# Optimization experiments

Measured on AMD Instinct MI355X. Metric: run time of the kernel, lower is better.

Reference implementation:

```python
import jax, jax.numpy as jnp
import numpy as np

HEADS = 8
DIM_HEAD = 64
SCALE = DIM_HEAD ** -0.5


def setup_inputs() -> dict:
    key = jax.random.key(0)
    ks = jax.random.split(key, 6)
    B, T, C, H, W = 16, 64, 512, 64, 64
    inner = HEADS * DIM_HEAD  # 512
    return {
        "vision_feature": jax.random.normal(ks[0], (B, C, H, W), jnp.float32),
        "language_feature": jax.random.normal(ks[1], (B, T, C), jnp.float32),
        "mask": jnp.ones((B, T), jnp.int32),  # unused by the module's forward
        "Wq": jax.random.normal(ks[2], (inner, C), jnp.float32) * (C ** -0.5),
        "Wk": jax.random.normal(ks[3], (inner, C), jnp.float32) * (C ** -0.5),
        "Wv": jax.random.normal(ks[4], (inner, C), jnp.float32) * (C ** -0.5),
        "Wo": jax.random.normal(ks[5], (C, inner), jnp.float32) * (inner ** -0.5),
    }


def reference(vision_feature, language_feature, mask, Wq, Wk, Wv, Wo):
    B, T, C = language_feature.shape
    _, _, H, W = vision_feature.shape
    S = H * W
    # 1x1 conv projections == matmuls over the channel dim
    q = jnp.einsum('btc,ic->bti', language_feature, Wq)           # (B, T, inner)
    vis = vision_feature.reshape(B, C, S)                          # (B, C, S)
    k = jnp.einsum('ic,bcs->bis', Wk, vis)                         # (B, inner, S)
    v = jnp.einsum('ic,bcs->bis', Wv, vis)                         # (B, inner, S)
    # split heads: channel index = n*dim_head + d  (n outermost)
    q = q.reshape(B, T, HEADS, DIM_HEAD).transpose(2, 0, 1, 3)     # (h, B, T, d)
    k = k.reshape(B, HEADS, DIM_HEAD, S).transpose(1, 0, 2, 3)     # (h, B, d, S)
    v = v.reshape(B, HEADS, DIM_HEAD, S).transpose(1, 0, 3, 2)     # (h, B, S, d)
    att = jax.nn.softmax(jnp.einsum('hbtd,hbds->hbts', q, k) * SCALE, axis=-1)
    out = jnp.einsum('hbts,hbsd->hbtd', att, v)                    # (h, B, T, d)
    # merge heads back: b (n c) tokens -> equivalently (B, T, h*d)
    out = out.transpose(1, 2, 0, 3).reshape(B, T, HEADS * DIM_HEAD)
    out = jnp.einsum('bti,oi->bto', out, Wo)                       # (B, T, C)
    return out
```

## Files before the change

### kernel.cpp

```cpp
#include <hip/hip_runtime.h>
#include <stdint.h>

typedef __attribute__((ext_vector_type(8))) short short8;
typedef __attribute__((ext_vector_type(4))) short short4v;
typedef __attribute__((ext_vector_type(4))) float float4v;
typedef __attribute__((ext_vector_type(8))) __bf16 bf16x8;

#define NCH 4

__device__ __forceinline__ float4v mfma16x16x32(short8 a, short8 b, float4v c) {
  return __builtin_amdgcn_mfma_f32_16x16x32_bf16(
      __builtin_bit_cast(bf16x8, a), __builtin_bit_cast(bf16x8, b), c, 0, 0, 0);
}

__device__ __forceinline__ short f2bf(float f) {
  uint32_t u = __builtin_bit_cast(uint32_t, f);
  u += 0x7fffu + ((u >> 16) & 1u);
  return (short)(u >> 16);
}

__device__ __forceinline__ float bf2f(short s) {
  return __builtin_bit_cast(float, ((uint32_t)(uint16_t)s) << 16);
}

__device__ __forceinline__ void load_lds16(const short* g, short* l) {
  __builtin_amdgcn_global_load_lds(
      (const __attribute__((address_space(1))) void*)g,
      (__attribute__((address_space(3))) void*)l, 16, 0, 0);
}

__global__ __launch_bounds__(256) void convert5(
    const float* __restrict__ sl, short* __restrict__ dl,
    const float* __restrict__ s1, short* __restrict__ d1,
    const float* __restrict__ s2, short* __restrict__ d2,
    const float* __restrict__ s3, short* __restrict__ d3,
    const float* __restrict__ s4, short* __restrict__ d4) {
  const float* src; short* dst; int n4;
  switch (blockIdx.y) {
    case 0: src = sl; dst = dl; n4 = 131072; break;
    case 1: src = s1; dst = d1; n4 = 65536; break;
    case 2: src = s2; dst = d2; n4 = 65536; break;
    case 3: src = s3; dst = d3; n4 = 65536; break;
    default: src = s4; dst = d4; n4 = 65536; break;
  }
  const int stride = gridDim.x * blockDim.x;
  for (int i = blockIdx.x * blockDim.x + threadIdx.x; i < n4; i += stride) {
    float4v v = *(const float4v*)(src + (long)i * 4);
    short4v o;
#pragma unroll
    for (int r = 0; r < 4; r++) o[r] = f2bf(v[r]);
    *(short4v*)(dst + (long)i * 4) = o;
  }
}

template <int OUT_F32>
__global__ __launch_bounds__(256) void gemm_nt(
    const short* __restrict__ A, const short* __restrict__ B,
    void* __restrict__ C, int K, int ldc, float scale) {
  __shared__ alignas(16) short lA[128 * 32];
  __shared__ alignas(16) short lB[128 * 32];
  const int tid = threadIdx.x;
  const int lane = tid & 63, w = tid >> 6;
  const int quad = lane >> 4, l16 = lane & 15;
  const int wm = w >> 1, wn = w & 1;
  const long m0 = (long)blockIdx.y * 128, n0 = (long)blockIdx.x * 128;

  float4v acc[4][4];
#pragma unroll
  for (int i = 0; i < 4; i++)
#pragma unroll
    for (int j = 0; j < 4; j++) acc[i][j] = (float4v)0.0f;

  const int srow = tid >> 2;
  const int scol = (tid & 3) * 8;

  for (int kt = 0; kt < K; kt += 32) {
    load_lds16(&A[(m0 + srow) * K + kt + scol], &lA[tid * 8]);
    load_lds16(&A[(m0 + 64 + srow) * K + kt + scol], &lA[2048 + tid * 8]);
    load_lds16(&B[(n0 + srow) * K + kt + scol], &lB[tid * 8]);
    load_lds16(&B[(n0 + 64 + srow) * K + kt + scol], &lB[2048 + tid * 8]);
    __syncthreads();

    short8 af[4], bf[4];
#pragma unroll
    for (int t = 0; t < 4; t++) {
      af[t] = *(const short8*)&lA[(wm * 64 + t * 16 + l16) * 32 + quad * 8];
      bf[t] = *(const short8*)&lB[(wn * 64 + t * 16 + l16) * 32 + quad * 8];
    }
#pragma unroll
    for (int i = 0; i < 4; i++)
#pragma unroll
      for (int j = 0; j < 4; j++)
        acc[i][j] = mfma16x16x32(af[i], bf[j], acc[i][j]);
    __syncthreads();
  }

  const int cm = wm * 64 + quad * 4;
  const int cn = wn * 64 + l16;
  if (OUT_F32) {
    float* Cf = (float*)C;
#pragma unroll
    for (int i = 0; i < 4; i++)
#pragma unroll
      for (int j = 0; j < 4; j++) {
        const long gn = n0 + cn + j * 16;
#pragma unroll
        for (int r = 0; r < 4; r++)
          Cf[(m0 + cm + i * 16 + r) * (long)ldc + gn] = acc[i][j][r] * scale;
      }
  } else {
    short* Cs = (short*)C;
#pragma unroll
    for (int i = 0; i < 4; i++)
#pragma unroll
      for (int j = 0; j < 4; j++) {
        const long gn = n0 + cn + j * 16;
#pragma unroll
        for (int r = 0; r < 4; r++)
          Cs[(m0 + cm + i * 16 + r) * (long)ldc + gn] = f2bf(acc[i][j][r] * scale);
      }
  }
}

__global__ __launch_bounds__(512) void gemm_kv(
    const short* __restrict__ Wk, const short* __restrict__ Wv,
    const short* __restrict__ visT, long sV,
    short* __restrict__ kout, short* __restrict__ vout, long sKV) {
  __shared__ alignas(16) short smem[12288];
  short* lWk = smem;
  short* lWv = smem + 4096;
  short* lVis = smem + 8192;
  const int tid = threadIdx.x;
  const int lane = tid & 63, w = tid >> 6;
  const int quad = lane >> 4, l16 = lane & 15;
  const int role = w >> 2;
  const int wq = w & 3, wm = wq >> 1, wn = wq & 1;
  const long n0 = (long)blockIdx.x * 128;
  const long m0 = (long)blockIdx.y * 128;
  const short* vis = visT + blockIdx.z * sV;
  short* kz = kout + blockIdx.z * sKV;
  short* vz = vout + blockIdx.z * sKV;

  float4v acc[4][4];
#pragma unroll
  for (int i = 0; i < 4; i++)
#pragma unroll
    for (int j = 0; j < 4; j++) acc[i][j] = (float4v)0.0f;

  const int srow = tid >> 2;
  const int scol = (tid & 3) * 8;
  const short* lW = role ? lWv : lWk;

  for (int kt = 0; kt < 512; kt += 32) {
    load_lds16(&Wk[(m0 + srow) * 512 + kt + scol], &lWk[tid * 8]);
    load_lds16(&Wv[(m0 + srow) * 512 + kt + scol], &lWv[tid * 8]);
    load_lds16(&vis[(n0 + srow) * 512 + kt + scol], &lVis[tid * 8]);
    __syncthreads();

    short8 af[4], bf[4];
#pragma unroll
    for (int t = 0; t < 4; t++) {
      af[t] = *(const short8*)&lW[(wm * 64 + t * 16 + l16) * 32 + quad * 8];
      bf[t] = *(const short8*)&lVis[(wn * 64 + t * 16 + l16) * 32 + quad * 8];
    }
#pragma unroll
    for (int i = 0; i < 4; i++)
#pragma unroll
      for (int j = 0; j < 4; j++)
        acc[i][j] = mfma16x16x32(af[i], bf[j], acc[i][j]);
    __syncthreads();
  }

  const int cm = wm * 64 + quad * 4;
  const int cn = wn * 64 + l16;

  if (role == 1) {
#pragma unroll
    for (int i = 0; i < 4; i++)
#pragma unroll
      for (int j = 0; j < 4; j++) {
        const long gn = n0 + cn + j * 16;
#pragma unroll
        for (int r = 0; r < 4; r++)
          vz[(m0 + cm + i * 16 + r) * 4096 + gn] = f2bf(acc[i][j][r]);
      }
  }

  short* scratch = smem;
#pragma unroll
  for (int h = 0; h < 2; h++) {
    __syncthreads();
    if (role == 0 && wn == h) {
#pragma unroll
      for (int j = 0; j < 4; j++)
#pragma unroll
        for (int i = 0; i < 4; i++) {
          const int nloc = j * 16 + l16;
          const int m = wm * 64 + i * 16 + quad * 4;
          short4v pk;
#pragma unroll
          for (int r = 0; r < 4; r++) pk[r] = f2bf(acc[i][j][r]);
          *(short4v*)&scratch[nloc * 136 + m] = pk;
        }
    }
    __syncthreads();
    {
      const int row = tid >> 3;
      const int off = (tid & 7) * 16;
      short8 v0 = *(const short8*)&scratch[row * 136 + off];
      short8 v1 = *(const short8*)&scratch[row * 136 + off + 8];
      *(short8*)&kz[(n0 + h * 64 + row) * 512 + m0 + off] = v0;
      *(short8*)&kz[(n0 + h * 64 + row) * 512 + m0 + off + 8] = v1;
    }
  }
}

__global__ __launch_bounds__(256) void transpose_f2b(
    const float* __restrict__ vis, short* __restrict__ visT) {
  __shared__ alignas(16) short buf[64][68];
  const int tid = threadIdx.x;
  const long bz = blockIdx.z;
  const long s0 = (long)blockIdx.x * 64;
  const long c0 = (long)blockIdx.y * 64;
  const float* src = vis + bz * 512 * 4096;
  short* dst = visT + bz * 4096 * 512;
  const int tr = tid >> 4;
  const int tc4 = (tid & 15) * 4;
#pragma unroll
  for (int i = 0; i < 4; i++) {
    const int c = tr + i * 16;
    float4v val = *(const float4v*)&src[(c0 + c) * 4096 + s0 + tc4];
    buf[tc4 + 0][c] = f2bf(val[0]);
    buf[tc4 + 1][c] = f2bf(val[1]);
    buf[tc4 + 2][c] = f2bf(val[2]);
    buf[tc4 + 3][c] = f2bf(val[3]);
  }
  __syncthreads();
#pragma unroll
  for (int i = 0; i < 4; i++) {
    const int s = tr + i * 16;
    short4v val = *(const short4v*)&buf[s][tc4];
    *(short4v*)&dst[(s0 + s) * 512 + c0 + tc4] = val;
  }
}

__global__ __launch_bounds__(256) void attn_part(
    const short* __restrict__ q, const short* __restrict__ kws,
    const short* __restrict__ vws, float* __restrict__ Opart,
    float* __restrict__ lpart, int b0) {
  const int h = blockIdx.x;
  const int bz = blockIdx.y;
  const int ch = blockIdx.z;
  const int tid = threadIdx.x;
  const int lane = tid & 63, w = tid >> 6;
  const int quad = lane >> 4, l16 = lane & 15;

  __shared__ alignas(16) short lq[64 * 64];
  __shared__ alignas(16) short lk[128 * 64];
  __shared__ alignas(16) short lv[64 * 128];
  __shared__ alignas(16) short lp[64 * 128];
  __shared__ float lsum[64];

  const short* qb = q + ((long)(b0 + bz) * 64) * 512 + h * 64;
  const short* kb = kws + (long)bz * 4096 * 512 + h * 64;
  const short* vb = vws + (long)bz * 512 * 4096 + (long)h * 64 * 4096;

  if (tid < 64) lsum[tid] = 0.0f;
  load_lds16(&qb[(tid >> 3) * 512 + (tid & 7) * 8], &lq[tid * 8]);
  load_lds16(&qb[(32 + (tid >> 3)) * 512 + (tid & 7) * 8], &lq[2048 + tid * 8]);
  __syncthreads();

  short8 aq[4][2];
#pragma unroll
  for (int mt = 0; mt < 4; mt++)
#pragma unroll
    for (int ks = 0; ks < 2; ks++)
      aq[mt][ks] = *(const short8*)&lq[(mt * 16 + l16) * 64 + ks * 32 + quad * 8];

  float4v osc[4];
#pragma unroll
  for (int mt = 0; mt < 4; mt++) osc[mt] = (float4v)0.0f;
  float lrow[4][4] = {};

  const int send = ch * (4096 / NCH) + (4096 / NCH);
  for (int s0 = ch * (4096 / NCH); s0 < send; s0 += 128) {
#pragma unroll
    for (int it = 0; it < 4; it++) {
      const int li = tid + it * 256;
      load_lds16(&kb[(long)(s0 + (li >> 3)) * 512 + (li & 7) * 8], &lk[li * 8]);
    }
#pragma unroll
    for (int it = 0; it < 4; it++) {
      const int li = tid + it * 256;
      load_lds16(&vb[(long)(li >> 4) * 4096 + s0 + (li & 15) * 8], &lv[li * 8]);
    }
    __syncthreads();

    float4v sc[4][2];
#pragma unroll
    for (int mt = 0; mt < 4; mt++)
#pragma unroll
      for (int jn = 0; jn < 2; jn++) sc[mt][jn] = (float4v)0.0f;
#pragma unroll
    for (int ks = 0; ks < 2; ks++) {
      short8 bk[2];
#pragma unroll
      for (int jn = 0; jn < 2; jn++)
        bk[jn] = *(const short8*)&lk[((2 * w + jn) * 16 + l16) * 64 + ks * 32 + quad * 8];
#pragma unroll
      for (int mt = 0; mt < 4; mt++)
#pragma unroll
        for (int jn = 0; jn < 2; jn++)
          sc[mt][jn] = mfma16x16x32(aq[mt][ks], bk[jn], sc[mt][jn]);
    }

#pragma unroll
    for (int mt = 0; mt < 4; mt++)
#pragma unroll
      for (int jn = 0; jn < 2; jn++)
#pragma unroll
        for (int r = 0; r < 4; r++) {
          const float scv = fminf(fmaxf(sc[mt][jn][r], -80.0f), 30.0f);
          const short sp = f2bf(__expf(scv));
          lrow[mt][r] += bf2f(sp);
          lp[(mt * 16 + quad * 4 + r) * 128 + (2 * w + jn) * 16 + l16] = sp;
        }
    __syncthreads();

#pragma unroll
    for (int ks = 0; ks < 4; ks++) {
      const short8 bv = *(const short8*)&lv[(w * 16 + l16) * 128 + ks * 32 + quad * 8];
#pragma unroll
      for (int mt = 0; mt < 4; mt++) {
        const short8 ap = *(const short8*)&lp[(mt * 16 + l16) * 128 + ks * 32 + quad * 8];
        osc[mt] = mfma16x16x32(ap, bv, osc[mt]);
      }
    }
    __syncthreads();
  }

#pragma unroll
  for (int mt = 0; mt < 4; mt++)
#pragma unroll
    for (int r = 0; r < 4; r++) {
      float v = lrow[mt][r];
      v += __shfl_xor(v, 1);
      v += __shfl_xor(v, 2);
      v += __shfl_xor(v, 4);
      v += __shfl_xor(v, 8);
      if (l16 == 0) atomicAdd(&lsum[mt * 16 + quad * 4 + r], v);
    }
  __syncthreads();

  const long bh = bz * 8 + h;
  float* op = Opart + ((bh * NCH + ch) * 64) * 64 + w * 16 + l16;
#pragma unroll
  for (int mt = 0; mt < 4; mt++)
#pragma unroll
    for (int r = 0; r < 4; r++)
      op[(long)(mt * 16 + quad * 4 + r) * 64] = osc[mt][r];
  if (tid < 64) lpart[(bh * NCH + ch) * 64 + tid] = lsum[tid];
}

__global__ __launch_bounds__(256) void attn_combine(
    const float* __restrict__ Opart, const float* __restrict__ lpart,
    short* __restrict__ tmp, int b0, int nbh) {
  const int total = nbh * 4096;
  for (int idx = blockIdx.x * 256 + threadIdx.x; idx < total;
       idx += gridDim.x * 256) {
    const int bh = idx >> 12;
    const int td = idx & 4095;
    const int t = td >> 6, d = td & 63;
    float o = 0.0f, l = 0.0f;
#pragma unroll
    for (int c = 0; c < NCH; c++) {
      o += Opart[((long)bh * NCH + c) * 4096 + td];
      l += lpart[(bh * NCH + c) * 64 + t];
    }
    const int b = b0 + (bh >> 3), h = bh & 7;
    tmp[((long)b * 64 + t) * 512 + h * 64 + d] = f2bf(o / l);
  }
}

extern "C" void kernel_launch(void* const* d_in, const int* in_sizes, int n_in,
                              void* d_out, int out_size, void* d_ws, size_t ws_size,
                              hipStream_t stream) {
  (void)in_sizes; (void)n_in; (void)out_size;
  const float* vis = (const float*)d_in[0];
  const float* lang = (const float*)d_in[1];
  const float* Wq = (const float*)d_in[3];
  const float* Wk = (const float*)d_in[4];
  const float* Wv = (const float*)d_in[5];
  const float* Wo = (const float*)d_in[6];
  float* out = (float*)d_out;

  char* ws = (char*)d_ws;
  const size_t MB = 1 << 20;
  short* q_ws = (short*)(ws + 0 * MB);
  short* tmp_ws = (short*)(ws + 1 * MB);
  short* langb = (short*)(ws + 2 * MB);
  short* Wqb = (short*)(ws + 3 * MB);
  short* Wkb = (short*)(ws + 3 * MB + 512 * 1024);
  short* Wvb = (short*)(ws + 4 * MB);
  short* Wob = (short*)(ws + 4 * MB + 512 * 1024);
  char* grp = ws + 5 * MB;

  const long batch_elems = 4096l * 512;
  int g = 16;
  const int cands[5] = {1, 2, 4, 8, 16};
  for (int ci = 0; ci < 5; ci++) {
    const size_t need = 5 * MB + 3ull * (16 / cands[ci]) * batch_elems * 2;
    if (need <= ws_size) { g = cands[ci]; break; }
  }
  const int Bg = 16 / g;
  short* visT = (short*)grp;
  short* k_ws = visT + (long)Bg * batch_elems;
  short* v_ws = k_ws + (long)Bg * batch_elems;
  float* Opart = (float*)visT;
  float* lptr = Opart + (long)Bg * 8 * NCH * 4096;

  convert5<<<dim3(128, 5), 256, 0, stream>>>(lang, langb, Wq, Wqb, Wk, Wkb,
                                             Wv, Wvb, Wo, Wob);

  gemm_nt<0><<<dim3(4, 8), 256, 0, stream>>>(langb, Wqb, q_ws, 512, 512, 0.125f);

  for (int gi = 0; gi < g; gi++) {
    const int b0 = gi * Bg;
    transpose_f2b<<<dim3(64, 8, Bg), 256, 0, stream>>>(vis + (long)b0 * batch_elems, visT);
    gemm_kv<<<dim3(32, 4, Bg), 512, 0, stream>>>(Wkb, Wvb, visT, batch_elems,
                                                 k_ws, v_ws, batch_elems);
    attn_part<<<dim3(8, Bg, NCH), 256, 0, stream>>>(q_ws, k_ws, v_ws, Opart, lptr, b0);
    attn_combine<<<512, 256, 0, stream>>>(Opart, lptr, tmp_ws, b0, Bg * 8);
  }

  gemm_nt<1><<<dim3(4, 8), 256, 0, stream>>>(tmp_ws, Wob, out, 512, 512, 1.0f);
}
```

Measured before the change: 406.9 us.

## Apply XOR swizzle to LDS tiles to remove bank conflicts

Adds an XOR-based column swizzle to every LDS tile (GEMM A/B tiles, K/V projection tiles, and the attention Q, K, V and P buffers). The global-to-LDS loads pick permuted source columns, and every fragment read or P write applies the same permutation, so the 16-byte fragment reads by lanes in a wavefront land in different LDS banks. The aim is to cut bank conflicts on the MFMA operand loads. It costs a few extra integer ops per address and needs every load and store to agree on the mapping.

```diff
diff --git a/kernel.cpp b/kernel.cpp
--- a/kernel.cpp
+++ b/kernel.cpp
@@ -72,7 +72,7 @@
     for (int j = 0; j < 4; j++) acc[i][j] = (float4v)0.0f;
 
   const int srow = tid >> 2;
-  const int scol = (tid & 3) * 8;
+  const int scol = (((tid & 3) ^ ((srow >> 1) & 3))) * 8;
 
   for (int kt = 0; kt < K; kt += 32) {
     load_lds16(&A[(m0 + srow) * K + kt + scol], &lA[tid * 8]);
@@ -84,8 +84,10 @@
     short8 af[4], bf[4];
 #pragma unroll
     for (int t = 0; t < 4; t++) {
-      af[t] = *(const short8*)&lA[(wm * 64 + t * 16 + l16) * 32 + quad * 8];
-      bf[t] = *(const short8*)&lB[(wn * 64 + t * 16 + l16) * 32 + quad * 8];
+      const int ra = wm * 64 + t * 16 + l16;
+      const int rb = wn * 64 + t * 16 + l16;
+      af[t] = *(const short8*)&lA[ra * 32 + ((quad ^ ((ra >> 1) & 3)) * 8)];
+      bf[t] = *(const short8*)&lB[rb * 32 + ((quad ^ ((rb >> 1) & 3)) * 8)];
     }
 #pragma unroll
     for (int i = 0; i < 4; i++)
@@ -148,7 +150,7 @@
     for (int j = 0; j < 4; j++) acc[i][j] = (float4v)0.0f;
 
   const int srow = tid >> 2;
-  const int scol = (tid & 3) * 8;
+  const int scol = (((tid & 3) ^ ((srow >> 1) & 3))) * 8;
   const short* lW = role ? lWv : lWk;
 
   for (int kt = 0; kt < 512; kt += 32) {
@@ -160,8 +162,10 @@
     short8 af[4], bf[4];
 #pragma unroll
     for (int t = 0; t < 4; t++) {
-      af[t] = *(const short8*)&lW[(wm * 64 + t * 16 + l16) * 32 + quad * 8];
-      bf[t] = *(const short8*)&lVis[(wn * 64 + t * 16 + l16) * 32 + quad * 8];
+      const int ra = wm * 64 + t * 16 + l16;
+      const int rb = wn * 64 + t * 16 + l16;
+      af[t] = *(const short8*)&lW[ra * 32 + ((quad ^ ((ra >> 1) & 3)) * 8)];
+      bf[t] = *(const short8*)&lVis[rb * 32 + ((quad ^ ((rb >> 1) & 3)) * 8)];
     }
 #pragma unroll
     for (int i = 0; i < 4; i++)
@@ -266,16 +270,22 @@
   const short* vb = vws + (long)bz * 512 * 4096 + (long)h * 64 * 4096;
 
   if (tid < 64) lsum[tid] = 0.0f;
-  load_lds16(&qb[(tid >> 3) * 512 + (tid & 7) * 8], &lq[tid * 8]);
-  load_lds16(&qb[(32 + (tid >> 3)) * 512 + (tid & 7) * 8], &lq[2048 + tid * 8]);
+  {
+    const int qr = tid >> 3;
+    const int qc = ((tid & 7) ^ (qr & 7)) * 8;
+    load_lds16(&qb[qr * 512 + qc], &lq[tid * 8]);
+    load_lds16(&qb[(32 + qr) * 512 + qc], &lq[2048 + tid * 8]);
+  }
   __syncthreads();
 
   short8 aq[4][2];
 #pragma unroll
   for (int mt = 0; mt < 4; mt++)
 #pragma unroll
-    for (int ks = 0; ks < 2; ks++)
-      aq[mt][ks] = *(const short8*)&lq[(mt * 16 + l16) * 64 + ks * 32 + quad * 8];
+    for (int ks = 0; ks < 2; ks++) {
+      const int ra = mt * 16 + l16;
+      aq[mt][ks] = *(const short8*)&lq[ra * 64 + (((ks * 4 + quad) ^ (ra & 7)) * 8)];
+    }
 
   float4v osc[4];
 #pragma unroll
@@ -287,12 +297,16 @@
 #pragma unroll
     for (int it = 0; it < 4; it++) {
       const int li = tid + it * 256;
-      load_lds16(&kb[(long)(s0 + (li >> 3)) * 512 + (li & 7) * 8], &lk[li * 8]);
+      const int kr = li >> 3;
+      const int kc = ((li & 7) ^ (kr & 7)) * 8;
+      load_lds16(&kb[(long)(s0 + kr) * 512 + kc], &lk[li * 8]);
     }
 #pragma unroll
     for (int it = 0; it < 4; it++) {
       const int li = tid + it * 256;
-      load_lds16(&vb[(long)(li >> 4) * 4096 + s0 + (li & 15) * 8], &lv[li * 8]);
+      const int vr = li >> 4;
+      const int vc = ((li & 15) ^ (vr & 7)) * 8;
+      load_lds16(&vb[(long)vr * 4096 + s0 + vc], &lv[li * 8]);
     }
     __syncthreads();
 
@@ -305,8 +319,10 @@
     for (int ks = 0; ks < 2; ks++) {
       short8 bk[2];
 #pragma unroll
-      for (int jn = 0; jn < 2; jn++)
-        bk[jn] = *(const short8*)&lk[((2 * w + jn) * 16 + l16) * 64 + ks * 32 + quad * 8];
+      for (int jn = 0; jn < 2; jn++) {
+        const int rb = (2 * w + jn) * 16 + l16;
+        bk[jn] = *(const short8*)&lk[rb * 64 + (((ks * 4 + quad) ^ (rb & 7)) * 8)];
+      }
 #pragma unroll
       for (int mt = 0; mt < 4; mt++)
 #pragma unroll
@@ -323,16 +339,20 @@
           const float scv = fminf(fmaxf(sc[mt][jn][r], -80.0f), 30.0f);
           const short sp = f2bf(__expf(scv));
           lrow[mt][r] += bf2f(sp);
-          lp[(mt * 16 + quad * 4 + r) * 128 + (2 * w + jn) * 16 + l16] = sp;
+          const int rowp = mt * 16 + quad * 4 + r;
+          const int col = (2 * w + jn) * 16 + l16;
+          lp[rowp * 128 + (((col >> 3) ^ (rowp & 7)) * 8) + (col & 7)] = sp;
         }
     __syncthreads();
 
 #pragma unroll
     for (int ks = 0; ks < 4; ks++) {
-      const short8 bv = *(const short8*)&lv[(w * 16 + l16) * 128 + ks * 32 + quad * 8];
+      const int rv = w * 16 + l16;
+      const short8 bv = *(const short8*)&lv[rv * 128 + (((ks * 4 + quad) ^ (rv & 7)) * 8)];
 #pragma unroll
       for (int mt = 0; mt < 4; mt++) {
-        const short8 ap = *(const short8*)&lp[(mt * 16 + l16) * 128 + ks * 32 + quad * 8];
+        const int rp = mt * 16 + l16;
+        const short8 ap = *(const short8*)&lp[rp * 128 + (((ks * 4 + quad) ^ (rp & 7)) * 8)];
         osc[mt] = mfma16x16x32(ap, bv, osc[mt]);
       }
     }
```

New measurement: 389.3 us. 1.05x faster.
